# Kernel optimization log

Measured on AMD Instinct MI355X. Metric: run time of the kernel, lower is better.

Reference implementation:

```python
import jax, jax.numpy as jnp
import numpy as np

ENCODED_DIM = 64
NUM_ENCODED = 512
BETA = 0.25


def setup_inputs() -> dict:
    key = jax.random.key(0)
    k1, k2 = jax.random.split(key)
    inputs = jax.random.normal(k1, (32, 64, 64, ENCODED_DIM), dtype=jnp.float32)
    # tf.random_uniform_initializer default: U[-0.05, 0.05]
    codebook = jax.random.uniform(k2, (ENCODED_DIM, NUM_ENCODED), dtype=jnp.float32,
                                  minval=-0.05, maxval=0.05)
    return {"inputs": inputs, "codebook": codebook}


def reference(inputs, codebook):
    original_shape = inputs.shape
    flat = inputs.reshape(-1, ENCODED_DIM)  # [N, D]
    # Squared Euclidean distances to each codebook column: [N, K]
    norms = (jnp.sum(flat ** 2, axis=1, keepdims=True)
             + jnp.sum(codebook ** 2, axis=0)
             - 2.0 * flat @ codebook)
    idx = jnp.argmin(norms, axis=1)  # [N]
    # one_hot @ codebook.T is exactly a row-gather of codebook.T
    quantized = jnp.take(codebook.T, idx, axis=0).reshape(original_shape)
    quantized_loss = jnp.mean((quantized - jax.lax.stop_gradient(inputs)) ** 2)
    commitment_loss = jnp.mean((jax.lax.stop_gradient(quantized) - inputs) ** 2)
    loss = BETA * commitment_loss + quantized_loss
    out = inputs + jax.lax.stop_gradient(quantized - inputs)
    return out, loss
```

## Files before the change

kernel.cpp:

```cpp
#include <hip/hip_runtime.h>
#include <math.h>

#define D 64
#define K 512
#define ROWS 131072
#define NELEM (ROWS * D)
#define T_FLAG 6e-5f
#define FLAGBIT (1 << 30)

typedef _Float16 half8 __attribute__((ext_vector_type(8)));
typedef float floatx4 __attribute__((ext_vector_type(4)));


__global__ __launch_bounds__(512) void vq_mfma(const float* __restrict__ x,
                                               const float* __restrict__ cb,
                                               float* __restrict__ out,
                                               double* __restrict__ loss_acc,
                                               int* __restrict__ counter,
                                               int* __restrict__ worklist) {
    __shared__ _Float16 cbH[32768];
    __shared__ _Float16 cbL[32768];
    __shared__ float ldsB[K];
    __shared__ int rowinfo[8][16];
    __shared__ float wavesum[8];

    const int tid = threadIdx.x;
    const int lane = tid & 63;
    const int w = tid >> 6;
    const int quad = lane >> 4;
    const int nn = lane & 15;

    for (int idx = tid; idx < 32768; idx += 512) {
        int k = idx >> 9, n = idx & 511;
        float c = cb[idx];
        float t = c * 4096.0f;
        _Float16 ch = (_Float16)t;
        float r = t - (float)ch;
        _Float16 cl = (_Float16)(r * 4096.0f);
        int off = (((n >> 4) * 2 + (k >> 5)) * 64
                   + ((k >> 3) & 3) * 16 + (n & 15)) * 8 + (k & 7);
        cbH[off] = ch;
        cbL[off] = cl;
    }
    {
#pragma clang fp contract(off)
        int j = tid;
        if (j < K) {
            float b = 0.f;
            for (int k = 0; k < D; ++k) { float c = cb[k * K + j]; b = b + c * c; }
            ldsB[j] = b;
        }
    }
    __syncthreads();

    const int rowBase = blockIdx.x * 128 + w * 16;

    half8 xh[2], xl[2];
    #pragma unroll
    for (int s = 0; s < 2; ++s) {
        const float* xp = x + (size_t)(rowBase + nn) * D + s * 32 + quad * 8;
        float4 v0 = *(const float4*)xp;
        float4 v1 = *(const float4*)(xp + 4);
        float vv[8] = {v0.x, v0.y, v0.z, v0.w, v1.x, v1.y, v1.z, v1.w};
        #pragma unroll
        for (int j = 0; j < 8; ++j) {
            float t = vv[j] * 256.0f;
            _Float16 h = (_Float16)t;
            float r = t - (float)h;
            xh[s][j] = h;
            xl[s][j] = (_Float16)(r * 4096.0f);
        }
    }

    float m1[4] = {INFINITY, INFINITY, INFINITY, INFINITY};
    float m2[4] = {INFINITY, INFINITY, INFINITY, INFINITY};
    int   i1[4] = {0, 0, 0, 0};

    #pragma unroll 4
    for (int t = 0; t < 32; ++t) {
        floatx4 acc1 = {0.f, 0.f, 0.f, 0.f};
        floatx4 acc2 = {0.f, 0.f, 0.f, 0.f};
        #pragma unroll
        for (int s = 0; s < 2; ++s) {
            int fo = (t * 2 + s) * 64 + lane;
            half8 bh = ((const half8*)cbH)[fo];
            half8 bl = ((const half8*)cbL)[fo];
            acc2 = __builtin_amdgcn_mfma_f32_16x16x32_f16(xl[s], bh, acc2, 0, 0, 0);
            acc2 = __builtin_amdgcn_mfma_f32_16x16x32_f16(xh[s], bl, acc2, 0, 0, 0);
            acc1 = __builtin_amdgcn_mfma_f32_16x16x32_f16(xh[s], bh, acc1, 0, 0, 0);
        }
        int col = t * 16 + nn;
        float Bj = ldsB[col];
        #pragma unroll
        for (int r = 0; r < 4; ++r) {
            float M = fmaf(0x1p-32f, acc2[r], 0x1p-20f * acc1[r]);
            float g = fmaf(-2.0f, M, Bj);
            bool c1 = g < m1[r];
            bool c2 = g < m2[r];
            m2[r] = c1 ? m1[r] : (c2 ? g : m2[r]);
            m1[r] = c1 ? g : m1[r];
            i1[r] = c1 ? col : i1[r];
        }
    }

    #pragma unroll
    for (int dlt = 1; dlt < 16; dlt <<= 1) {
        #pragma unroll
        for (int r = 0; r < 4; ++r) {
            float om1 = __shfl_xor(m1[r], dlt);
            int   oi1 = __shfl_xor(i1[r], dlt);
            float om2 = __shfl_xor(m2[r], dlt);
            bool ofirst = (om1 < m1[r]) || (om1 == m1[r] && oi1 < i1[r]);
            float l1   = ofirst ? m1[r] : om1;
            float cand = ofirst ? om2 : m2[r];
            m1[r] = ofirst ? om1 : m1[r];
            i1[r] = ofirst ? oi1 : i1[r];
            m2[r] = fminf(cand, l1);
        }
    }

    if (nn == 0) {
        #pragma unroll
        for (int r = 0; r < 4; ++r) {
            bool flg = (m2[r] - m1[r]) < T_FLAG;
            rowinfo[w][quad * 4 + r] = i1[r] | (flg ? FLAGBIT : 0);
            if (flg) {
                int pos = atomicAdd(counter, 1);
                worklist[pos] = rowBase + quad * 4 + r;
            }
        }
    }
    __syncthreads();

    float lsum = 0.f;
    #pragma unroll
    for (int p = 0; p < 4; ++p) {
        int rl = p * 4 + quad;
        int info = rowinfo[w][rl];
        if (!(info & FLAGBIT)) {
            int j = info & 511;
            int kb = nn * 4;
            float q0 = cb[(kb + 0) * K + j];
            float q1 = cb[(kb + 1) * K + j];
            float q2 = cb[(kb + 2) * K + j];
            float q3 = cb[(kb + 3) * K + j];
            size_t row = (size_t)rowBase + rl;
            float4 xv = *(const float4*)(x + row * D + kb);
            float e0 = q0 - xv.x, e1 = q1 - xv.y, e2 = q2 - xv.z, e3 = q3 - xv.w;
            lsum += e0 * e0 + e1 * e1 + e2 * e2 + e3 * e3;
            *(float4*)(out + row * D + kb) = make_float4(q0, q1, q2, q3);
        }
    }
    #pragma unroll
    for (int off = 32; off > 0; off >>= 1) lsum += __shfl_down(lsum, off);
    if (lane == 0) wavesum[w] = lsum;
    __syncthreads();
    if (tid == 0) {
        double tot = 0.0;
        #pragma unroll
        for (int i = 0; i < 8; ++i) tot += (double)wavesum[i];
        atomicAdd(loss_acc, tot);
    }
}

__global__ __launch_bounds__(256) void vq_rescan(const float* __restrict__ x,
                                                 const float* __restrict__ cb,
                                                 float* __restrict__ out,
                                                 double* __restrict__ loss_acc,
                                                 const int* __restrict__ counter,
                                                 const int* __restrict__ worklist) {
#pragma clang fp contract(off)
    const int lane = threadIdx.x & 63;
    const int gwave = blockIdx.x * 4 + (threadIdx.x >> 6);
    const int nwaves = gridDim.x * 4;
    const int count = *counter;

    for (int idx = gwave; idx < count; idx += nwaves) {
        int row = __builtin_amdgcn_readfirstlane(worklist[idx]);
        const float* xr = x + (size_t)row * D;

        float A0;
        {
            float rr[8];
            #pragma unroll
            for (int l = 0; l < 8; ++l) rr[l] = xr[l] * xr[l];
            #pragma unroll
            for (int m = 1; m < 8; ++m)
                #pragma unroll
                for (int l = 0; l < 8; ++l) {
                    float q = xr[8 * m + l] * xr[8 * m + l];
                    rr[l] = rr[l] + q;
                }
            A0 = ((rr[0] + rr[1]) + (rr[2] + rr[3])) + ((rr[4] + rr[5]) + (rr[6] + rr[7]));
        }

        float a[8], b[8];
        #pragma unroll
        for (int m = 0; m < 8; ++m) { a[m] = 0.f; b[m] = 0.f; }
        for (int k = 0; k < D; ++k) {
            float xk = xr[k];
            const float* crow = cb + k * K + lane;
            #pragma unroll
            for (int m = 0; m < 8; ++m) {
                float c = crow[m * 64];
                a[m] = fmaf(xk, c, a[m]);
                b[m] = b[m] + c * c;
            }
        }
        float db = INFINITY; int jb = 0x7fffffff;
        #pragma unroll
        for (int m = 0; m < 8; ++m) {
            float s = A0 + b[m];
            float t2 = 2.0f * a[m];
            float d = s - t2;
            int j = lane + (m << 6);
            if (d < db) { db = d; jb = j; }
        }
        for (int s = 1; s < 64; s <<= 1) {
            float od = __shfl_xor(db, s);
            int oj = __shfl_xor(jb, s);
            if ((od < db) || (od == db && oj < jb)) { db = od; jb = oj; }
        }
        float q = cb[lane * K + jb];
        out[(size_t)row * D + lane] = q;
        float e = q - xr[lane];
        float ls = e * e;
        #pragma unroll
        for (int off = 32; off > 0; off >>= 1) ls += __shfl_down(ls, off);
        if (lane == 0) atomicAdd(loss_acc, (double)ls);
    }
}

__global__ void vq_finalize(const double* __restrict__ acc, float* __restrict__ out) {
    out[NELEM] = (float)(acc[0] * (1.25 / (double)NELEM));
}

extern "C" void kernel_launch(void* const* d_in, const int* in_sizes, int n_in,
                              void* d_out, int out_size, void* d_ws, size_t ws_size,
                              hipStream_t stream) {
    const float* x  = (const float*)d_in[0];
    const float* cb = (const float*)d_in[1];
    float* out = (float*)d_out;
    double* loss_acc = (double*)d_ws;
    int* counter = (int*)((char*)d_ws + 8);
    int* worklist = (int*)((char*)d_ws + 16);

    hipMemsetAsync(d_ws, 0, 16, stream);
    vq_mfma<<<ROWS / 128, 512, 0, stream>>>(x, cb, out, loss_acc, counter, worklist);
    vq_rescan<<<512, 256, 0, stream>>>(x, cb, out, loss_acc, counter, worklist);
    vq_finalize<<<1, 1, 0, stream>>>(loss_acc, out);
}
```

Before: 186.7 us.

## Precompute split-fp16 codebook once, stream from global, 64 rows per wave, bitmap rescan

The codebook hi/lo fp16 split and norm computation moves out of every block into a small setup kernel that writes a pre-swizzled copy to workspace. The main kernel streams codebook fragments from global/L2 instead of staging 128KB in LDS per block, and each wave now handles 64 rows (four 16-row tiles) so every loaded B fragment feeds four MFMA groups. The flag threshold is rescaled to match the new accumulation scaling. Near-tie rows are recorded in a per-block bitmap instead of an atomic worklist, and the rescan hoists codebook norms per wave. This raises register pressure and relies on L2 bandwidth for the codebook reads.

```diff
diff --git a/kernel.cpp b/kernel.cpp
--- a/kernel.cpp
+++ b/kernel.cpp
@@ -5,24 +5,48 @@
 #define K 512
 #define ROWS 131072
 #define NELEM (ROWS * D)
-#define T_FLAG 6e-5f
+#define TGAP 64.0f
 #define FLAGBIT (1 << 30)
 
 typedef _Float16 half8 __attribute__((ext_vector_type(8)));
 typedef float floatx4 __attribute__((ext_vector_type(4)));
 
 
-__global__ __launch_bounds__(512) void vq_mfma(const float* __restrict__ x,
-                                               const float* __restrict__ cb,
-                                               float* __restrict__ out,
-                                               double* __restrict__ loss_acc,
-                                               int* __restrict__ counter,
-                                               int* __restrict__ worklist) {
-    __shared__ _Float16 cbH[32768];
-    __shared__ _Float16 cbL[32768];
+__global__ __launch_bounds__(512) void vq_setup(const float* __restrict__ cb,
+                                                _Float16* __restrict__ gH,
+                                                _Float16* __restrict__ gL,
+                                                float* __restrict__ Bn) {
+    int idx = blockIdx.x * 512 + threadIdx.x;
+    int k = idx >> 9, n = idx & 511;
+    float c = cb[idx];
+    float t = c * 4096.0f;
+    _Float16 ch = (_Float16)t;
+    float r = t - (float)ch;
+    _Float16 cl = (_Float16)(r * 4096.0f);
+    int off = (((n >> 4) * 2 + (k >> 5)) * 64 + ((k >> 3) & 3) * 16 + (n & 15)) * 8 + (k & 7);
+    gH[off] = ch;
+    gL[off] = cl;
+    if (blockIdx.x == 0) {
+#pragma clang fp contract(off)
+        int j = threadIdx.x;
+        float b = 0.f;
+        for (int kk = 0; kk < D; ++kk) { float cc = cb[kk * K + j]; b = b + cc * cc; }
+        Bn[j] = b * 0x1p20f;
+    }
+}
+
+__global__ __launch_bounds__(256, 2) void vq_main(const float* __restrict__ x,
+                                                  const float* __restrict__ cb,
+                                                  const _Float16* __restrict__ gH,
+                                                  const _Float16* __restrict__ gL,
+                                                  const float* __restrict__ Bn,
+                                                  float* __restrict__ out,
+                                                  double* __restrict__ loss_acc,
+                                                  unsigned int* __restrict__ bitmap) {
     __shared__ float ldsB[K];
-    __shared__ int rowinfo[8][16];
-    __shared__ float wavesum[8];
+    __shared__ int rowinfo[4][64];
+    __shared__ unsigned int flagbits[8];
+    __shared__ float wavesum[4];
 
     const int tid = threadIdx.x;
     const int lane = tid & 63;
@@ -30,125 +54,126 @@
     const int quad = lane >> 4;
     const int nn = lane & 15;
 
-    for (int idx = tid; idx < 32768; idx += 512) {
-        int k = idx >> 9, n = idx & 511;
-        float c = cb[idx];
-        float t = c * 4096.0f;
-        _Float16 ch = (_Float16)t;
-        float r = t - (float)ch;
-        _Float16 cl = (_Float16)(r * 4096.0f);
-        int off = (((n >> 4) * 2 + (k >> 5)) * 64
-                   + ((k >> 3) & 3) * 16 + (n & 15)) * 8 + (k & 7);
-        cbH[off] = ch;
-        cbL[off] = cl;
-    }
-    {
-#pragma clang fp contract(off)
-        int j = tid;
-        if (j < K) {
-            float b = 0.f;
-            for (int k = 0; k < D; ++k) { float c = cb[k * K + j]; b = b + c * c; }
-            ldsB[j] = b;
+    ldsB[tid] = Bn[tid];
+    ldsB[tid + 256] = Bn[tid + 256];
+    if (tid < 8) flagbits[tid] = 0;
+
+    const int rowBase = blockIdx.x * 256 + w * 64;
+
+    half8 xh[4][2], xl[4][2];
+    #pragma unroll
+    for (int tt = 0; tt < 4; ++tt) {
+        #pragma unroll
+        for (int s = 0; s < 2; ++s) {
+            const float* xp = x + (size_t)(rowBase + tt * 16 + nn) * D + s * 32 + quad * 8;
+            float4 v0 = *(const float4*)xp;
+            float4 v1 = *(const float4*)(xp + 4);
+            float vv[8] = {v0.x, v0.y, v0.z, v0.w, v1.x, v1.y, v1.z, v1.w};
+            #pragma unroll
+            for (int j = 0; j < 8; ++j) {
+                float t = vv[j] * 256.0f;
+                _Float16 h = (_Float16)t;
+                float r = t - (float)h;
+                xh[tt][s][j] = h;
+                xl[tt][s][j] = (_Float16)(r * 4096.0f);
+            }
         }
     }
     __syncthreads();
 
-    const int rowBase = blockIdx.x * 128 + w * 16;
-
-    half8 xh[2], xl[2];
-    #pragma unroll
-    for (int s = 0; s < 2; ++s) {
-        const float* xp = x + (size_t)(rowBase + nn) * D + s * 32 + quad * 8;
-        float4 v0 = *(const float4*)xp;
-        float4 v1 = *(const float4*)(xp + 4);
-        float vv[8] = {v0.x, v0.y, v0.z, v0.w, v1.x, v1.y, v1.z, v1.w};
-        #pragma unroll
-        for (int j = 0; j < 8; ++j) {
-            float t = vv[j] * 256.0f;
-            _Float16 h = (_Float16)t;
-            float r = t - (float)h;
-            xh[s][j] = h;
-            xl[s][j] = (_Float16)(r * 4096.0f);
-        }
-    }
-
-    float m1[4] = {INFINITY, INFINITY, INFINITY, INFINITY};
-    float m2[4] = {INFINITY, INFINITY, INFINITY, INFINITY};
-    int   i1[4] = {0, 0, 0, 0};
-
-    #pragma unroll 4
+    float m1[4][4], m2[4][4];
+    int   i1[4][4];
+    #pragma unroll
+    for (int tt = 0; tt < 4; ++tt)
+        #pragma unroll
+        for (int r = 0; r < 4; ++r) { m1[tt][r] = INFINITY; m2[tt][r] = INFINITY; i1[tt][r] = 0; }
+
+    const half8* bHp = (const half8*)gH;
+    const half8* bLp = (const half8*)gL;
+
+    #pragma unroll 2
     for (int t = 0; t < 32; ++t) {
-        floatx4 acc1 = {0.f, 0.f, 0.f, 0.f};
-        floatx4 acc2 = {0.f, 0.f, 0.f, 0.f};
-        #pragma unroll
-        for (int s = 0; s < 2; ++s) {
-            int fo = (t * 2 + s) * 64 + lane;
-            half8 bh = ((const half8*)cbH)[fo];
-            half8 bl = ((const half8*)cbL)[fo];
-            acc2 = __builtin_amdgcn_mfma_f32_16x16x32_f16(xl[s], bh, acc2, 0, 0, 0);
-            acc2 = __builtin_amdgcn_mfma_f32_16x16x32_f16(xh[s], bl, acc2, 0, 0, 0);
-            acc1 = __builtin_amdgcn_mfma_f32_16x16x32_f16(xh[s], bh, acc1, 0, 0, 0);
-        }
+        half8 bh0 = bHp[(t * 2 + 0) * 64 + lane];
+        half8 bl0 = bLp[(t * 2 + 0) * 64 + lane];
+        half8 bh1 = bHp[(t * 2 + 1) * 64 + lane];
+        half8 bl1 = bLp[(t * 2 + 1) * 64 + lane];
         int col = t * 16 + nn;
         float Bj = ldsB[col];
         #pragma unroll
-        for (int r = 0; r < 4; ++r) {
-            float M = fmaf(0x1p-32f, acc2[r], 0x1p-20f * acc1[r]);
-            float g = fmaf(-2.0f, M, Bj);
-            bool c1 = g < m1[r];
-            bool c2 = g < m2[r];
-            m2[r] = c1 ? m1[r] : (c2 ? g : m2[r]);
-            m1[r] = c1 ? g : m1[r];
-            i1[r] = c1 ? col : i1[r];
+        for (int tt = 0; tt < 4; ++tt) {
+            floatx4 a1 = {0.f, 0.f, 0.f, 0.f};
+            floatx4 a2 = {0.f, 0.f, 0.f, 0.f};
+            a2 = __builtin_amdgcn_mfma_f32_16x16x32_f16(xl[tt][0], bh0, a2, 0, 0, 0);
+            a2 = __builtin_amdgcn_mfma_f32_16x16x32_f16(xh[tt][0], bl0, a2, 0, 0, 0);
+            a1 = __builtin_amdgcn_mfma_f32_16x16x32_f16(xh[tt][0], bh0, a1, 0, 0, 0);
+            a2 = __builtin_amdgcn_mfma_f32_16x16x32_f16(xl[tt][1], bh1, a2, 0, 0, 0);
+            a2 = __builtin_amdgcn_mfma_f32_16x16x32_f16(xh[tt][1], bl1, a2, 0, 0, 0);
+            a1 = __builtin_amdgcn_mfma_f32_16x16x32_f16(xh[tt][1], bh1, a1, 0, 0, 0);
+            #pragma unroll
+            for (int r = 0; r < 4; ++r) {
+                float macc = fmaf(0x1p-12f, a2[r], a1[r]);
+                float g = fmaf(-2.0f, macc, Bj);
+                float old1 = m1[tt][r];
+                bool c1 = g < old1;
+                m2[tt][r] = fminf(fmaxf(g, old1), m2[tt][r]);
+                m1[tt][r] = c1 ? g : old1;
+                i1[tt][r] = c1 ? col : i1[tt][r];
+            }
         }
     }
 
     #pragma unroll
     for (int dlt = 1; dlt < 16; dlt <<= 1) {
         #pragma unroll
-        for (int r = 0; r < 4; ++r) {
-            float om1 = __shfl_xor(m1[r], dlt);
-            int   oi1 = __shfl_xor(i1[r], dlt);
-            float om2 = __shfl_xor(m2[r], dlt);
-            bool ofirst = (om1 < m1[r]) || (om1 == m1[r] && oi1 < i1[r]);
-            float l1   = ofirst ? m1[r] : om1;
-            float cand = ofirst ? om2 : m2[r];
-            m1[r] = ofirst ? om1 : m1[r];
-            i1[r] = ofirst ? oi1 : i1[r];
-            m2[r] = fminf(cand, l1);
-        }
+        for (int tt = 0; tt < 4; ++tt)
+            #pragma unroll
+            for (int r = 0; r < 4; ++r) {
+                float om1 = __shfl_xor(m1[tt][r], dlt);
+                int   oi1 = __shfl_xor(i1[tt][r], dlt);
+                float om2 = __shfl_xor(m2[tt][r], dlt);
+                bool ofirst = (om1 < m1[tt][r]) || (om1 == m1[tt][r] && oi1 < i1[tt][r]);
+                float l1   = ofirst ? m1[tt][r] : om1;
+                float cand = ofirst ? om2 : m2[tt][r];
+                m1[tt][r] = ofirst ? om1 : m1[tt][r];
+                i1[tt][r] = ofirst ? oi1 : i1[tt][r];
+                m2[tt][r] = fminf(cand, l1);
+            }
     }
 
     if (nn == 0) {
         #pragma unroll
-        for (int r = 0; r < 4; ++r) {
-            bool flg = (m2[r] - m1[r]) < T_FLAG;
-            rowinfo[w][quad * 4 + r] = i1[r] | (flg ? FLAGBIT : 0);
-            if (flg) {
-                int pos = atomicAdd(counter, 1);
-                worklist[pos] = rowBase + quad * 4 + r;
-            }
-        }
+        for (int tt = 0; tt < 4; ++tt)
+            #pragma unroll
+            for (int r = 0; r < 4; ++r) {
+                int rl = tt * 16 + quad * 4 + r;
+                bool flg = (m2[tt][r] - m1[tt][r]) < TGAP;
+                rowinfo[w][rl] = i1[tt][r] | (flg ? FLAGBIT : 0);
+                if (flg) atomicOr(&flagbits[(w * 64 + rl) >> 5], 1u << ((w * 64 + rl) & 31));
+            }
     }
     __syncthreads();
+    if (tid < 8) bitmap[blockIdx.x * 8 + tid] = flagbits[tid];
 
     float lsum = 0.f;
     #pragma unroll
-    for (int p = 0; p < 4; ++p) {
-        int rl = p * 4 + quad;
-        int info = rowinfo[w][rl];
-        if (!(info & FLAGBIT)) {
-            int j = info & 511;
-            int kb = nn * 4;
-            float q0 = cb[(kb + 0) * K + j];
-            float q1 = cb[(kb + 1) * K + j];
-            float q2 = cb[(kb + 2) * K + j];
-            float q3 = cb[(kb + 3) * K + j];
-            size_t row = (size_t)rowBase + rl;
-            float4 xv = *(const float4*)(x + row * D + kb);
-            float e0 = q0 - xv.x, e1 = q1 - xv.y, e2 = q2 - xv.z, e3 = q3 - xv.w;
-            lsum += e0 * e0 + e1 * e1 + e2 * e2 + e3 * e3;
-            *(float4*)(out + row * D + kb) = make_float4(q0, q1, q2, q3);
+    for (int tt = 0; tt < 4; ++tt) {
+        #pragma unroll
+        for (int p = 0; p < 4; ++p) {
+            int rl = tt * 16 + p * 4 + quad;
+            int info = rowinfo[w][rl];
+            if (!(info & FLAGBIT)) {
+                int j = info & 511;
+                int kb = nn * 4;
+                float q0 = cb[(kb + 0) * K + j];
+                float q1 = cb[(kb + 1) * K + j];
+                float q2 = cb[(kb + 2) * K + j];
+                float q3 = cb[(kb + 3) * K + j];
+                size_t row = (size_t)rowBase + rl;
+                float4 xv = *(const float4*)(x + row * D + kb);
+                float e0 = q0 - xv.x, e1 = q1 - xv.y, e2 = q2 - xv.z, e3 = q3 - xv.w;
+                lsum += e0 * e0 + e1 * e1 + e2 * e2 + e3 * e3;
+                *(float4*)(out + row * D + kb) = make_float4(q0, q1, q2, q3);
+            }
         }
     }
     #pragma unroll
@@ -156,9 +181,8 @@
     if (lane == 0) wavesum[w] = lsum;
     __syncthreads();
     if (tid == 0) {
-        double tot = 0.0;
-        #pragma unroll
-        for (int i = 0; i < 8; ++i) tot += (double)wavesum[i];
+        double tot = (double)wavesum[0] + (double)wavesum[1]
+                   + (double)wavesum[2] + (double)wavesum[3];
         atomicAdd(loss_acc, tot);
     }
 }
@@ -167,68 +191,79 @@
                                                  const float* __restrict__ cb,
                                                  float* __restrict__ out,
                                                  double* __restrict__ loss_acc,
-                                                 const int* __restrict__ counter,
-                                                 const int* __restrict__ worklist) {
+                                                 const unsigned int* __restrict__ bitmap) {
 #pragma clang fp contract(off)
     const int lane = threadIdx.x & 63;
     const int gwave = blockIdx.x * 4 + (threadIdx.x >> 6);
-    const int nwaves = gridDim.x * 4;
-    const int count = *counter;
-
-    for (int idx = gwave; idx < count; idx += nwaves) {
-        int row = __builtin_amdgcn_readfirstlane(worklist[idx]);
-        const float* xr = x + (size_t)row * D;
-
-        float A0;
-        {
-            float rr[8];
-            #pragma unroll
-            for (int l = 0; l < 8; ++l) rr[l] = xr[l] * xr[l];
-            #pragma unroll
-            for (int m = 1; m < 8; ++m)
-                #pragma unroll
-                for (int l = 0; l < 8; ++l) {
-                    float q = xr[8 * m + l] * xr[8 * m + l];
-                    rr[l] = rr[l] + q;
-                }
-            A0 = ((rr[0] + rr[1]) + (rr[2] + rr[3])) + ((rr[4] + rr[5]) + (rr[6] + rr[7]));
-        }
-
-        float a[8], b[8];
-        #pragma unroll
-        for (int m = 0; m < 8; ++m) { a[m] = 0.f; b[m] = 0.f; }
+
+    unsigned int w0 = bitmap[gwave * 2 + 0];
+    unsigned int w1 = bitmap[gwave * 2 + 1];
+    unsigned long long mask = ((unsigned long long)w1 << 32) | w0;
+    float wloss = 0.f;
+    if (mask) {
+        float bn[8];
+        #pragma unroll
+        for (int m = 0; m < 8; ++m) bn[m] = 0.f;
         for (int k = 0; k < D; ++k) {
-            float xk = xr[k];
             const float* crow = cb + k * K + lane;
             #pragma unroll
             for (int m = 0; m < 8; ++m) {
                 float c = crow[m * 64];
-                a[m] = fmaf(xk, c, a[m]);
-                b[m] = b[m] + c * c;
-            }
-        }
-        float db = INFINITY; int jb = 0x7fffffff;
-        #pragma unroll
-        for (int m = 0; m < 8; ++m) {
-            float s = A0 + b[m];
-            float t2 = 2.0f * a[m];
-            float d = s - t2;
-            int j = lane + (m << 6);
-            if (d < db) { db = d; jb = j; }
-        }
-        for (int s = 1; s < 64; s <<= 1) {
-            float od = __shfl_xor(db, s);
-            int oj = __shfl_xor(jb, s);
-            if ((od < db) || (od == db && oj < jb)) { db = od; jb = oj; }
-        }
-        float q = cb[lane * K + jb];
-        out[(size_t)row * D + lane] = q;
-        float e = q - xr[lane];
-        float ls = e * e;
-        #pragma unroll
-        for (int off = 32; off > 0; off >>= 1) ls += __shfl_down(ls, off);
-        if (lane == 0) atomicAdd(loss_acc, (double)ls);
-    }
+                bn[m] = bn[m] + c * c;
+            }
+        }
+        while (mask) {
+            int b = __builtin_ctzll(mask);
+            mask &= mask - 1;
+            int row = gwave * 64 + b;
+            const float* xr = x + (size_t)row * D;
+            float A0;
+            {
+                float rr[8];
+                #pragma unroll
+                for (int l = 0; l < 8; ++l) rr[l] = xr[l] * xr[l];
+                #pragma unroll
+                for (int m = 1; m < 8; ++m)
+                    #pragma unroll
+                    for (int l = 0; l < 8; ++l) {
+                        float q = xr[8 * m + l] * xr[8 * m + l];
+                        rr[l] = rr[l] + q;
+                    }
+                A0 = ((rr[0] + rr[1]) + (rr[2] + rr[3])) + ((rr[4] + rr[5]) + (rr[6] + rr[7]));
+            }
+            float a[8];
+            #pragma unroll
+            for (int m = 0; m < 8; ++m) a[m] = 0.f;
+            for (int k = 0; k < D; ++k) {
+                float xk = xr[k];
+                const float* crow = cb + k * K + lane;
+                #pragma unroll
+                for (int m = 0; m < 8; ++m)
+                    a[m] = fmaf(xk, crow[m * 64], a[m]);
+            }
+            float db = INFINITY; int jb = 0x7fffffff;
+            #pragma unroll
+            for (int m = 0; m < 8; ++m) {
+                float s = A0 + bn[m];
+                float t2 = 2.0f * a[m];
+                float d = s - t2;
+                int j = lane + (m << 6);
+                if (d < db) { db = d; jb = j; }
+            }
+            for (int s = 1; s < 64; s <<= 1) {
+                float od = __shfl_xor(db, s);
+                int oj = __shfl_xor(jb, s);
+                if ((od < db) || (od == db && oj < jb)) { db = od; jb = oj; }
+            }
+            float q = cb[lane * K + jb];
+            out[(size_t)row * D + lane] = q;
+            float e = q - xr[lane];
+            wloss += e * e;
+        }
+    }
+    #pragma unroll
+    for (int off = 32; off > 0; off >>= 1) wloss += __shfl_down(wloss, off);
+    if (lane == 0 && wloss != 0.f) atomicAdd(loss_acc, (double)wloss);
 }
 
 __global__ void vq_finalize(const double* __restrict__ acc, float* __restrict__ out) {
@@ -242,11 +277,14 @@
     const float* cb = (const float*)d_in[1];
     float* out = (float*)d_out;
     double* loss_acc = (double*)d_ws;
-    int* counter = (int*)((char*)d_ws + 8);
-    int* worklist = (int*)((char*)d_ws + 16);
+    float* Bn        = (float*)((char*)d_ws + 4096);
+    _Float16* gH     = (_Float16*)((char*)d_ws + 8192);
+    _Float16* gL     = (_Float16*)((char*)d_ws + 73728);
+    unsigned int* bm = (unsigned int*)((char*)d_ws + 139264);
 
     hipMemsetAsync(d_ws, 0, 16, stream);
-    vq_mfma<<<ROWS / 128, 512, 0, stream>>>(x, cb, out, loss_acc, counter, worklist);
-    vq_rescan<<<512, 256, 0, stream>>>(x, cb, out, loss_acc, counter, worklist);
+    vq_setup<<<64, 512, 0, stream>>>(cb, gH, gL, Bn);
+    vq_main<<<ROWS / 256, 256, 0, stream>>>(x, cb, gH, gL, Bn, out, loss_acc, bm);
+    vq_rescan<<<512, 256, 0, stream>>>(x, cb, out, loss_acc, bm);
     vq_finalize<<<1, 1, 0, stream>>>(loss_acc, out);
 }
```

Measured after the change: 176.7 us. -5.4%, faster.
